# Optimization experiments

Hardware: AMD Instinct MI355X
Metric: run time of the kernel (lower is better)

The kernel has to match this reference:

```python
import jax, jax.numpy as jnp
import numpy as np

HEADS = 16
DIM_HEAD = 64


def rotate_half(t):
    x1, x2 = jnp.split(t, 2, axis=-1)
    return jnp.concatenate((-x2, x1), axis=-1)


def apply_rotary_pos_emb(t, freqs):
    # t: [b, h, n, l], freqs: [n, l]
    seq_len = t.shape[-2]
    freqs = freqs[-seq_len:, :]
    return t * jnp.cos(freqs) + rotate_half(t) * jnp.sin(freqs)


def setup_inputs() -> dict:
    key = jax.random.key(0)
    ks = jax.random.split(key, 6)
    b, n, dim, l = 2, 2048, 1024, 32
    x = jax.random.normal(ks[0], (b, n, dim), dtype=jnp.float32)
    rotary_pos_emb = jax.random.normal(ks[1], (n, l), dtype=jnp.float32)
    s = 0.02
    Wq = jax.random.normal(ks[2], (dim, dim), dtype=jnp.float32) * s
    Wk = jax.random.normal(ks[3], (dim, dim), dtype=jnp.float32) * s
    Wv = jax.random.normal(ks[4], (dim, dim), dtype=jnp.float32) * s
    Wout = jax.random.normal(ks[5], (dim, dim), dtype=jnp.float32) * s
    return {"x": x, "rotary_pos_emb": rotary_pos_emb, "Wq": Wq, "Wk": Wk, "Wv": Wv, "Wout": Wout}


def reference(x, rotary_pos_emb, Wq, Wk, Wv, Wout):
    b, n, _ = x.shape
    h, d = HEADS, DIM_HEAD
    scale = d ** -0.5

    def to_heads(t):
        return t.reshape(b, n, h, d).transpose(0, 2, 1, 3)  # b h n d

    q = to_heads(x @ Wq)
    k = to_heads(x @ Wk)
    v = to_heads(x @ Wv)

    # partial rotary on first l dims of q, k, v (module applies rope to v too)
    l = rotary_pos_emb.shape[-1]

    def rope(t):
        tl, tr = t[..., :l], t[..., l:]
        return jnp.concatenate((apply_rotary_pos_emb(tl, rotary_pos_emb), tr), axis=-1)

    q, k, v = rope(q), rope(k), rope(v)

    dots = jnp.einsum('bhid,bhjd->bhij', q, k) * scale  # [b, h, n, n]
    mask_value = jnp.finfo(dots.dtype).min
    causal = jnp.triu(jnp.ones((n, n), dtype=bool), k=1)  # i < j
    dots = jnp.where(causal[None, None, :, :], mask_value, dots)

    attn = jax.nn.softmax(dots, axis=-1)
    out = jnp.einsum('bhij,bhjd->bhid', attn, v)
    out = out.transpose(0, 2, 1, 3).reshape(b, n, h * d)  # b n (h d)
    return out @ Wout
```

## Files before the change

kernel.cpp:

```cpp
#include <hip/hip_runtime.h>
#include <hip/hip_bf16.h>
#include <stdint.h>

#define BATCH 2
#define SEQ 2048
#define NHEADS 16
#define DIM 1024
#define MTOT 4096
#define LOG2E 1.4426950408889634f
#define QSCALE (0.125f * LOG2E)
#define DEFER_THR 11.54f

typedef __attribute__((ext_vector_type(8))) short s16x8;
typedef __attribute__((ext_vector_type(4))) float f32x4;
typedef unsigned short u16;

__device__ __forceinline__ u16 f2b(float f) {
  union { float f; uint32_t u; } v; v.f = f;
  uint32_t r = v.u + 0x7FFFu + ((v.u >> 16) & 1u);
  return (u16)(r >> 16);
}
__device__ __forceinline__ u16 f2b_fast(float f) {
  union { float f; uint32_t u; } v; v.f = f;
  return (u16)((v.u + 0x8000u) >> 16);
}
__device__ __forceinline__ float b2f(u16 h) {
  union { uint32_t u; float f; } v; v.u = ((uint32_t)h) << 16;
  return v.f;
}

__device__ __forceinline__ void gload_lds16(void* lds, const void* g) {
  __builtin_amdgcn_global_load_lds(
      (const __attribute__((address_space(1))) unsigned int*)g,
      (__attribute__((address_space(3))) unsigned int*)lds, 16, 0, 0);
}

__global__ __launch_bounds__(256) void prep_kernel(
    const float* __restrict__ x, const float* __restrict__ Wq,
    const float* __restrict__ Wk, const float* __restrict__ Wv,
    const float* __restrict__ Wo, const float* __restrict__ rot,
    u16* __restrict__ xb, u16* __restrict__ WtAll, float2* __restrict__ cs) {
  __shared__ float tile[32][33];
  int bid = blockIdx.x, t = threadIdx.x;
  if (bid < 4096) {
    int i = (bid * 256 + t) * 4;
    float4 v = *(const float4*)(x + i);
    ushort4 o;
    o.x = f2b(v.x); o.y = f2b(v.y); o.z = f2b(v.z); o.w = f2b(v.w);
    *(ushort4*)(xb + i) = o;
  } else if (bid < 8192) {
    int bb = bid - 4096;
    int z = bb >> 10, xB = bb & 31, yB = (bb >> 5) & 31;
    const float* W = (z == 0) ? Wq : (z == 1) ? Wk : (z == 2) ? Wv : Wo;
    u16* Wt = WtAll + (size_t)z * DIM * DIM;
    int k0 = xB * 32, n0 = yB * 32;
    int tx = t & 31, ty = t >> 5;
#pragma unroll
    for (int i = 0; i < 4; i++) {
      int r = ty + i * 8;
      tile[r][tx] = W[(size_t)(k0 + r) * DIM + n0 + tx];
    }
    __syncthreads();
#pragma unroll
    for (int i = 0; i < 4; i++) {
      int r = ty + i * 8;
      Wt[(size_t)(n0 + r) * DIM + k0 + tx] = f2b(tile[tx][r]);
    }
  } else {
    int i = (bid - 8192) * 256 + t;
    float f = rot[i];
    float s, c;
    __sincosf(f, &s, &c);
    cs[i] = make_float2(c, s);
  }
}

#define NKT 16
__global__ __launch_bounds__(512, 2) void qkv8_kernel(
    const u16* __restrict__ A, const u16* __restrict__ Bt,
    const float2* __restrict__ cs, u16* __restrict__ Qh,
    u16* __restrict__ Kh, u16* __restrict__ Vt) {
  __shared__ u16 lds[2][4][8192];
  const int t = threadIdx.x;
  const int w = t >> 6, l = t & 63;
  const int wr = w >> 2, wc = w & 3;
  const int lr = l & 15, lg = l >> 4;
  const int rowBase = blockIdx.x * 256;
  const int colBase = blockIdx.y * 256;
  const char* Ab = (const char*)(A + (size_t)rowBase * DIM);
  const char* Bb = (const char*)(Bt + (size_t)colBase * DIM);
  const int t16 = t * 16;
  const int swz = ((lr >> 1) & 3) << 4;

  f32x4 acc[8][4];
#pragma unroll
  for (int m = 0; m < 8; m++)
#pragma unroll
    for (int n = 0; n < 4; n++) acc[m][n] = (f32x4){0.f, 0.f, 0.f, 0.f};

  auto stageH = [&](int buf, int kind, int kt) {
    const char* gb = (kind >= 2) ? Bb : Ab;
    int khalf = kind & 1;
    char* ldst = (char*)&lds[buf][kind][0];
#pragma unroll
    for (int i = 0; i < 2; i++) {
      int ob = t16 + i * 8192;
      int row = ob >> 6, cb = ob & 63;
      gload_lds16(ldst + ob,
                  gb + (size_t)row * (DIM * 2) + kt * 128 + khalf * 64 +
                      (cb ^ (((row >> 1) & 3) << 4)));
    }
  };
  auto rdA = [&](int cur, int m, int kk) -> s16x8 {
    int R = wr * 128 + m * 16 + lr;
    return *(const s16x8*)((const char*)&lds[cur][kk][0] + R * 64 + ((lg * 16) ^ swz));
  };
  auto rdB = [&](int cur, int n, int kk) -> s16x8 {
    int R = wc * 64 + n * 16 + lr;
    return *(const s16x8*)((const char*)&lds[cur][2 + kk][0] + R * 64 + ((lg * 16) ^ swz));
  };

  stageH(0, 0, 0); stageH(0, 2, 0); stageH(0, 1, 0); stageH(0, 3, 0);
  stageH(1, 2, 1); stageH(1, 0, 1); stageH(1, 3, 1);

  for (int kt = 0; kt < NKT; ++kt) {
    const int cur = kt & 1, nxt = cur ^ 1;
    if (kt >= NKT - 2) { asm volatile("s_waitcnt vmcnt(0)" ::: "memory"); }
    else               { asm volatile("s_waitcnt vmcnt(6)" ::: "memory"); }
    __builtin_amdgcn_s_barrier();
    __builtin_amdgcn_sched_barrier(0);

    s16x8 af[4], bf[4];
#pragma unroll
    for (int i = 0; i < 4; i++) { af[i] = rdA(cur, i, 0); bf[i] = rdB(cur, i, 0); }
    if (kt + 1 < NKT) stageH(nxt, 1, kt + 1);
    __builtin_amdgcn_s_barrier();
    __builtin_amdgcn_sched_barrier(0);
    __builtin_amdgcn_s_setprio(1);
#pragma unroll
    for (int m = 0; m < 4; m++)
#pragma unroll
      for (int n = 0; n < 4; n++)
        acc[m][n] = __builtin_amdgcn_mfma_f32_16x16x32_bf16(af[m], bf[n], acc[m][n], 0, 0, 0);
    __builtin_amdgcn_s_setprio(0);
    __builtin_amdgcn_s_barrier();
    __builtin_amdgcn_sched_barrier(0);
#pragma unroll
    for (int i = 0; i < 4; i++) af[i] = rdA(cur, 4 + i, 0);
    if (kt + 2 < NKT) stageH(cur, 2, kt + 2);
    __builtin_amdgcn_s_barrier();
    __builtin_amdgcn_sched_barrier(0);
    __builtin_amdgcn_s_setprio(1);
#pragma unroll
    for (int m = 0; m < 4; m++)
#pragma unroll
      for (int n = 0; n < 4; n++)
        acc[4 + m][n] = __builtin_amdgcn_mfma_f32_16x16x32_bf16(af[m], bf[n], acc[4 + m][n], 0, 0, 0);
    __builtin_amdgcn_s_setprio(0);
    __builtin_amdgcn_s_barrier();
    __builtin_amdgcn_sched_barrier(0);
#pragma unroll
    for (int i = 0; i < 4; i++) { af[i] = rdA(cur, i, 1); bf[i] = rdB(cur, i, 1); }
    if (kt + 2 < NKT) stageH(cur, 0, kt + 2);
    __builtin_amdgcn_s_barrier();
    __builtin_amdgcn_sched_barrier(0);
    __builtin_amdgcn_s_setprio(1);
#pragma unroll
    for (int m = 0; m < 4; m++)
#pragma unroll
      for (int n = 0; n < 4; n++)
        acc[m][n] = __builtin_amdgcn_mfma_f32_16x16x32_bf16(af[m], bf[n], acc[m][n], 0, 0, 0);
    __builtin_amdgcn_s_setprio(0);
    __builtin_amdgcn_s_barrier();
    __builtin_amdgcn_sched_barrier(0);
#pragma unroll
    for (int i = 0; i < 4; i++) af[i] = rdA(cur, 4 + i, 1);
    if (kt + 2 < NKT) stageH(cur, 3, kt + 2);
    __builtin_amdgcn_s_barrier();
    __builtin_amdgcn_sched_barrier(0);
    __builtin_amdgcn_s_setprio(1);
#pragma unroll
    for (int m = 0; m < 4; m++)
#pragma unroll
      for (int n = 0; n < 4; n++)
        acc[4 + m][n] = __builtin_amdgcn_mfma_f32_16x16x32_bf16(af[m], bf[n], acc[4 + m][n], 0, 0, 0);
    __builtin_amdgcn_s_setprio(0);
    __builtin_amdgcn_s_barrier();
    __builtin_amdgcn_sched_barrier(0);
  }

  int cg = colBase + wc * 64;
  int z = cg >> 10;
  int h = (cg >> 6) & (NHEADS - 1);
  if (z == 2) {
#pragma unroll
    for (int m = 0; m < 8; m++) {
#pragma unroll
      for (int r = 0; r < 4; r++) {
        int row = rowBase + wr * 128 + m * 16 + lg * 4 + r;
        int nrow = row & (SEQ - 1);
        int b2 = row >> 11;
        const float2* csr = cs + (size_t)nrow * 32;
        float a0 = acc[m][0][r], a1 = acc[m][1][r];
        float2 f0 = csr[lr];
        float2 f1 = csr[16 + lr];
        float o0 = a0 * f0.x - a1 * f0.y;
        float o1 = a1 * f1.x + a0 * f1.y;
        size_t vbase = ((size_t)(b2 * NHEADS + h) * 64) * SEQ + nrow;
        Vt[vbase + (size_t)lr * SEQ]        = f2b(o0);
        Vt[vbase + (size_t)(16 + lr) * SEQ] = f2b(o1);
        Vt[vbase + (size_t)(32 + lr) * SEQ] = f2b(acc[m][2][r]);
        Vt[vbase + (size_t)(48 + lr) * SEQ] = f2b(acc[m][3][r]);
      }
    }
  } else {
    u16* C = (z == 0) ? Qh : Kh;
    float sc = (z == 0) ? QSCALE : 1.0f;
#pragma unroll
    for (int m = 0; m < 8; m++) {
#pragma unroll
      for (int r = 0; r < 4; r++) {
        int row = rowBase + wr * 128 + m * 16 + lg * 4 + r;
        int nrow = row & (SEQ - 1);
        int b2 = row >> 11;
        const float2* csr = cs + (size_t)nrow * 32;
        float a0 = acc[m][0][r], a1 = acc[m][1][r];
        float2 f0 = csr[lr];
        float2 f1 = csr[16 + lr];
        float o0 = (a0 * f0.x - a1 * f0.y) * sc;
        float o1 = (a1 * f1.x + a0 * f1.y) * sc;
        size_t base = ((size_t)(b2 * NHEADS + h) * SEQ + nrow) * 64;
        C[base + lr]      = f2b(o0);
        C[base + 16 + lr] = f2b(o1);
        C[base + 32 + lr] = f2b(acc[m][2][r] * sc);
        C[base + 48 + lr] = f2b(acc[m][3][r] * sc);
      }
    }
  }
}

__global__ __launch_bounds__(256) void gemm_out(
    const u16* __restrict__ A, const u16* __restrict__ Bt,
    float* __restrict__ C) {
  __shared__ u16 Asm[2][128 * 32];
  __shared__ u16 Bsm[2][128 * 32];
  int t = threadIdx.x;
  int w = t >> 6, l = t & 63;
  int wr = w >> 1, wc = w & 1;
  int lr = l & 15, lg = l >> 4;
  int rowBase = blockIdx.x * 128;
  int colBase = blockIdx.y * 128;
  const char* Ab = (const char*)(A + (size_t)rowBase * DIM);
  const char* Bb = (const char*)(Bt + (size_t)colBase * DIM);

  f32x4 acc[4][4];
#pragma unroll
  for (int m = 0; m < 4; m++)
#pragma unroll
    for (int n = 0; n < 4; n++) acc[m][n] = (f32x4){0.f, 0.f, 0.f, 0.f};

  auto stage = [&](int buf, int kt) {
#pragma unroll
    for (int i = 0; i < 2; i++) {
      int ob = t * 16 + i * 4096;
      int row = ob >> 6, cb = ob & 63;
      int src = row * (DIM * 2) + kt * 64 + (cb ^ (((row >> 1) & 3) << 4));
      gload_lds16((char*)&Asm[buf][0] + ob, Ab + src);
      gload_lds16((char*)&Bsm[buf][0] + ob, Bb + src);
    }
  };

  stage(0, 0);
  for (int kt = 0; kt < DIM / 32; ++kt) {
    int cur = kt & 1;
    __syncthreads();
    if (kt + 1 < DIM / 32) stage(cur ^ 1, kt + 1);
    const char* ab = (const char*)&Asm[cur][0];
    const char* bb = (const char*)&Bsm[cur][0];
    s16x8 af[4], bf[4];
#pragma unroll
    for (int m = 0; m < 4; m++) {
      int R = wr * 64 + m * 16 + lr;
      af[m] = *(const s16x8*)(ab + R * 64 + ((lg * 16) ^ (((R >> 1) & 3) << 4)));
    }
#pragma unroll
    for (int n = 0; n < 4; n++) {
      int R = wc * 64 + n * 16 + lr;
      bf[n] = *(const s16x8*)(bb + R * 64 + ((lg * 16) ^ (((R >> 1) & 3) << 4)));
    }
    __builtin_amdgcn_s_setprio(1);
#pragma unroll
    for (int m = 0; m < 4; m++)
#pragma unroll
      for (int n = 0; n < 4; n++)
        acc[m][n] = __builtin_amdgcn_mfma_f32_16x16x32_bf16(af[m], bf[n], acc[m][n], 0, 0, 0);
    __builtin_amdgcn_s_setprio(0);
  }

#pragma unroll
  for (int m = 0; m < 4; m++)
#pragma unroll
    for (int n = 0; n < 4; n++) {
      int row = rowBase + wr * 64 + m * 16 + lg * 4;
      int col = colBase + wc * 64 + n * 16 + lr;
#pragma unroll
      for (int r = 0; r < 4; r++)
        C[(size_t)(row + r) * DIM + col] = acc[m][n][r];
    }
}

__global__ __launch_bounds__(256) void attn_kernel(
    const u16* __restrict__ Qh, const u16* __restrict__ Kh,
    const u16* __restrict__ Vtg, u16* __restrict__ Ob) {
  int id = blockIdx.x;
  int xcd = id & 7, within = id >> 3;
  int bh = xcd * 4 + (within >> 4);
  int pi = within & 15;
  int b = bh >> 4, h = bh & 15;
  __shared__ u16 Ks[2][64 * 64];
  __shared__ u16 Vs[2][64 * 64];
  __shared__ u16 Ps[4][16 * 64];
  int t = threadIdx.x, w = t >> 6, l = t & 63;
  int lr = l & 15, lg = l >> 4;
  char* psb = (char*)&Ps[w][0];

  const char* Kbh = (const char*)(Kh + (size_t)bh * SEQ * 64);
  const char* Vbh = (const char*)Vtg + (size_t)bh * 64 * SEQ * 2;
  const u16* Qbh = Qh + (size_t)bh * SEQ * 64;

  auto stage = [&](int buf, int kt) {
    const char* kg = Kbh + (size_t)kt * 64 * 128;
    const char* vg = Vbh + kt * 128;
#pragma unroll
    for (int i = 0; i < 2; i++) {
      int ob = i * 4096 + t * 16;
      int row = ob >> 7, cb = ob & 127;
      int sw = cb ^ ((row & 7) << 4);
      gload_lds16((char*)&Ks[buf][0] + ob, kg + row * 128 + sw);
      gload_lds16((char*)&Vs[buf][0] + ob, vg + row * 4096 + sw);
    }
  };

#pragma unroll 1
  for (int ph = 0; ph < 2; ++ph) {
    int qt = ph ? (31 - pi) : pi;
    int nkt = qt + 1;
    int qrow0 = qt * 64 + w * 16;

    s16x8 qf[2];
#pragma unroll
    for (int kk = 0; kk < 2; kk++)
      qf[kk] = *(const s16x8*)(Qbh + (size_t)(qrow0 + lr) * 64 + kk * 32 + lg * 8);

    f32x4 o[4];
#pragma unroll
    for (int n = 0; n < 4; n++) o[n] = (f32x4){0.f, 0.f, 0.f, 0.f};
    float mrun[4], lsum[4];
#pragma unroll
    for (int r = 0; r < 4; r++) { mrun[r] = -3.0e38f; lsum[r] = 0.f; }

    __syncthreads();
    stage(0, 0);
    for (int kt = 0; kt < nkt; ++kt) {
      int cur = kt & 1;
      __syncthreads();
      if (kt + 1 < nkt) stage(cur ^ 1, kt + 1);
      const char* kb = (const char*)&Ks[cur][0];
      const char* vb = (const char*)&Vs[cur][0];

      f32x4 s[4];
#pragma unroll
      for (int n = 0; n < 4; n++) s[n] = (f32x4){0.f, 0.f, 0.f, 0.f};
      __builtin_amdgcn_s_setprio(1);
#pragma unroll
      for (int n = 0; n < 4; n++)
#pragma unroll
        for (int kk = 0; kk < 2; kk++) {
          int R = n * 16 + lr;
          s16x8 bk = *(const s16x8*)(kb + R * 128 + ((kk * 64 + lg * 16) ^ ((R & 7) << 4)));
          s[n] = __builtin_amdgcn_mfma_f32_16x16x32_bf16(qf[kk], bk, s[n], 0, 0, 0);
        }
      __builtin_amdgcn_s_setprio(0);

      if (kt == nkt - 1) {
#pragma unroll
        for (int n = 0; n < 4; n++) {
          int colg = kt * 64 + n * 16 + lr;
#pragma unroll
          for (int r = 0; r < 4; r++) {
            int rowg = qt * 64 + w * 16 + lg * 4 + r;
            if (colg > rowg) s[n][r] = -3.0e38f;
          }
        }
      }

      float tl[4];
#pragma unroll
      for (int r = 0; r < 4; r++)
        tl[r] = fmaxf(fmaxf(s[0][r], s[1][r]), fmaxf(s[2][r], s[3][r]));
      float need = fmaxf(fmaxf(tl[0] - mrun[0], tl[1] - mrun[1]),
                         fmaxf(tl[2] - mrun[2], tl[3] - mrun[3]));
      if (!__all(need <= DEFER_THR)) {
        float tm[4];
#pragma unroll
        for (int r = 0; r < 4; r++) tm[r] = tl[r];
#pragma unroll
        for (int off = 1; off < 16; off <<= 1)
#pragma unroll
          for (int r = 0; r < 4; r++) tm[r] = fmaxf(tm[r], __shfl_xor(tm[r], off, 64));
        float alpha[4];
#pragma unroll
        for (int r = 0; r < 4; r++) {
          float mn = fmaxf(mrun[r], tm[r]);
          alpha[r] = exp2f(mrun[r] - mn);
          mrun[r] = mn;
          lsum[r] *= alpha[r];
        }
#pragma unroll
        for (int n = 0; n < 4; n++)
#pragma unroll
          for (int r = 0; r < 4; r++) o[n][r] *= alpha[r];
      }
#pragma unroll
      for (int n = 0; n < 4; n++) {
#pragma unroll
        for (int r = 0; r < 4; r++) {
          float p = exp2f(s[n][r] - mrun[r]);
          lsum[r] += p;
          int prow = lg * 4 + r;
          *(u16*)(psb + prow * 128 + (((n * 16 + lr) * 2) ^ ((prow & 7) << 4))) = f2b_fast(p);
        }
      }

      s16x8 pa[2];
#pragma unroll
      for (int kk = 0; kk < 2; kk++)
        pa[kk] = *(const s16x8*)(psb + lr * 128 + ((kk * 64 + lg * 16) ^ ((lr & 7) << 4)));
      __builtin_amdgcn_s_setprio(1);
#pragma unroll
      for (int n = 0; n < 4; n++)
#pragma unroll
        for (int kk = 0; kk < 2; kk++) {
          int R = n * 16 + lr;
          s16x8 vv = *(const s16x8*)(vb + R * 128 + ((kk * 64 + lg * 16) ^ ((R & 7) << 4)));
          o[n] = __builtin_amdgcn_mfma_f32_16x16x32_bf16(pa[kk], vv, o[n], 0, 0, 0);
        }
      __builtin_amdgcn_s_setprio(0);
    }

#pragma unroll
    for (int off = 1; off < 16; off <<= 1)
#pragma unroll
      for (int r = 0; r < 4; r++) lsum[r] += __shfl_xor(lsum[r], off, 64);
    float inv[4];
#pragma unroll
    for (int r = 0; r < 4; r++) inv[r] = 1.0f / lsum[r];
#pragma unroll
    for (int n = 0; n < 4; n++)
#pragma unroll
      for (int r = 0; r < 4; r++) {
        int rowg = qt * 64 + w * 16 + lg * 4 + r;
        int col = h * 64 + n * 16 + lr;
        Ob[((size_t)b * SEQ + rowg) * DIM + col] = f2b(o[n][r] * inv[r]);
      }
  }
}

extern "C" void kernel_launch(void* const* d_in, const int* in_sizes, int n_in,
                              void* d_out, int out_size, void* d_ws, size_t ws_size,
                              hipStream_t stream) {
  (void)in_sizes; (void)n_in; (void)out_size; (void)ws_size;
  const float* x = (const float*)d_in[0];
  const float* rot = (const float*)d_in[1];
  const float* Wq = (const float*)d_in[2];
  const float* Wk = (const float*)d_in[3];
  const float* Wv = (const float*)d_in[4];
  const float* Wo = (const float*)d_in[5];

  char* ws = (char*)d_ws;
  u16* xb    = (u16*)(ws);
  u16* WtAll = (u16*)(ws + (8ll << 20));
  u16* Qh    = (u16*)(ws + (16ll << 20));
  u16* Kh    = (u16*)(ws + (24ll << 20));
  u16* Vt    = (u16*)(ws + (32ll << 20));
  u16* Ob    = (u16*)(ws + (40ll << 20));
  float2* cs = (float2*)(ws + (48ll << 20));

  prep_kernel<<<8448, 256, 0, stream>>>(x, Wq, Wk, Wv, Wo, rot, xb, WtAll, cs);
  qkv8_kernel<<<dim3(16, 12), 512, 0, stream>>>(xb, WtAll, cs, Qh, Kh, Vt);
  attn_kernel<<<512, 256, 0, stream>>>(Qh, Kh, Vt, Ob);
  gemm_out<<<dim3(32, 8), 256, 0, stream>>>(Ob, WtAll + 3ll * DIM * DIM, (float*)d_out);
}
```

Before: 199.5 us.

## Compute transposed scores in attention to keep P in registers; halve out-GEMM row tile

The attention kernel now computes S^T (K as the A operand), so each lane holds scores for a single query row. The row max and sum then need only two cross-lane shuffles, and P can be packed with v_cvt_pk_bf16 and fed straight into 16x16x16 MFMAs against V without the LDS round-trip. This drops the per-wave P shared buffer and its writes, reads and swizzle math, at the cost of twice as many smaller MFMAs for the PV product. The output GEMM tile shrinks from 128x128 to 64x128, doubling the grid to 512 blocks to fill more CUs, which trades away some operand reuse.

```diff
diff --git a/kernel.cpp b/kernel.cpp
--- a/kernel.cpp
+++ b/kernel.cpp
@@ -12,6 +12,7 @@
 #define DEFER_THR 11.54f
 
 typedef __attribute__((ext_vector_type(8))) short s16x8;
+typedef __attribute__((ext_vector_type(4))) short s16x4;
 typedef __attribute__((ext_vector_type(4))) float f32x4;
 typedef unsigned short u16;
 
@@ -20,13 +21,14 @@
   uint32_t r = v.u + 0x7FFFu + ((v.u >> 16) & 1u);
   return (u16)(r >> 16);
 }
-__device__ __forceinline__ u16 f2b_fast(float f) {
-  union { float f; uint32_t u; } v; v.f = f;
-  return (u16)((v.u + 0x8000u) >> 16);
-}
 __device__ __forceinline__ float b2f(u16 h) {
   union { uint32_t u; float f; } v; v.u = ((uint32_t)h) << 16;
   return v.f;
+}
+__device__ __forceinline__ uint32_t cvtpk_bf16(float a, float b) {
+  uint32_t r;
+  asm("v_cvt_pk_bf16_f32 %0, %1, %2" : "=v"(r) : "v"(a), "v"(b));
+  return r;
 }
 
 __device__ __forceinline__ void gload_lds16(void* lds, const void* g) {
@@ -242,31 +244,36 @@
 __global__ __launch_bounds__(256) void gemm_out(
     const u16* __restrict__ A, const u16* __restrict__ Bt,
     float* __restrict__ C) {
-  __shared__ u16 Asm[2][128 * 32];
+  __shared__ u16 Asm[2][64 * 32];
   __shared__ u16 Bsm[2][128 * 32];
   int t = threadIdx.x;
   int w = t >> 6, l = t & 63;
   int wr = w >> 1, wc = w & 1;
   int lr = l & 15, lg = l >> 4;
-  int rowBase = blockIdx.x * 128;
+  int rowBase = blockIdx.x * 64;
   int colBase = blockIdx.y * 128;
   const char* Ab = (const char*)(A + (size_t)rowBase * DIM);
   const char* Bb = (const char*)(Bt + (size_t)colBase * DIM);
 
-  f32x4 acc[4][4];
-#pragma unroll
-  for (int m = 0; m < 4; m++)
+  f32x4 acc[2][4];
+#pragma unroll
+  for (int m = 0; m < 2; m++)
 #pragma unroll
     for (int n = 0; n < 4; n++) acc[m][n] = (f32x4){0.f, 0.f, 0.f, 0.f};
 
   auto stage = [&](int buf, int kt) {
+    {
+      int ob = t * 16;
+      int row = ob >> 6, cb = ob & 63;
+      gload_lds16((char*)&Asm[buf][0] + ob,
+                  Ab + (size_t)row * (DIM * 2) + kt * 64 + (cb ^ (((row >> 1) & 3) << 4)));
+    }
 #pragma unroll
     for (int i = 0; i < 2; i++) {
       int ob = t * 16 + i * 4096;
       int row = ob >> 6, cb = ob & 63;
-      int src = row * (DIM * 2) + kt * 64 + (cb ^ (((row >> 1) & 3) << 4));
-      gload_lds16((char*)&Asm[buf][0] + ob, Ab + src);
-      gload_lds16((char*)&Bsm[buf][0] + ob, Bb + src);
+      gload_lds16((char*)&Bsm[buf][0] + ob,
+                  Bb + (size_t)row * (DIM * 2) + kt * 64 + (cb ^ (((row >> 1) & 3) << 4)));
     }
   };
 
@@ -277,10 +284,10 @@
     if (kt + 1 < DIM / 32) stage(cur ^ 1, kt + 1);
     const char* ab = (const char*)&Asm[cur][0];
     const char* bb = (const char*)&Bsm[cur][0];
-    s16x8 af[4], bf[4];
-#pragma unroll
-    for (int m = 0; m < 4; m++) {
-      int R = wr * 64 + m * 16 + lr;
+    s16x8 af[2], bf[4];
+#pragma unroll
+    for (int m = 0; m < 2; m++) {
+      int R = wr * 32 + m * 16 + lr;
       af[m] = *(const s16x8*)(ab + R * 64 + ((lg * 16) ^ (((R >> 1) & 3) << 4)));
     }
 #pragma unroll
@@ -290,7 +297,7 @@
     }
     __builtin_amdgcn_s_setprio(1);
 #pragma unroll
-    for (int m = 0; m < 4; m++)
+    for (int m = 0; m < 2; m++)
 #pragma unroll
       for (int n = 0; n < 4; n++)
         acc[m][n] = __builtin_amdgcn_mfma_f32_16x16x32_bf16(af[m], bf[n], acc[m][n], 0, 0, 0);
@@ -298,10 +305,10 @@
   }
 
 #pragma unroll
-  for (int m = 0; m < 4; m++)
+  for (int m = 0; m < 2; m++)
 #pragma unroll
     for (int n = 0; n < 4; n++) {
-      int row = rowBase + wr * 64 + m * 16 + lg * 4;
+      int row = rowBase + wr * 32 + m * 16 + lg * 4;
       int col = colBase + wc * 64 + n * 16 + lr;
 #pragma unroll
       for (int r = 0; r < 4; r++)
@@ -319,10 +326,8 @@
   int b = bh >> 4, h = bh & 15;
   __shared__ u16 Ks[2][64 * 64];
   __shared__ u16 Vs[2][64 * 64];
-  __shared__ u16 Ps[4][16 * 64];
   int t = threadIdx.x, w = t >> 6, l = t & 63;
   int lr = l & 15, lg = l >> 4;
-  char* psb = (char*)&Ps[w][0];
 
   const char* Kbh = (const char*)(Kh + (size_t)bh * SEQ * 64);
   const char* Vbh = (const char*)Vtg + (size_t)bh * 64 * SEQ * 2;
@@ -345,19 +350,17 @@
   for (int ph = 0; ph < 2; ++ph) {
     int qt = ph ? (31 - pi) : pi;
     int nkt = qt + 1;
-    int qrow0 = qt * 64 + w * 16;
+    int qrow = qt * 64 + w * 16 + lr;
 
     s16x8 qf[2];
 #pragma unroll
     for (int kk = 0; kk < 2; kk++)
-      qf[kk] = *(const s16x8*)(Qbh + (size_t)(qrow0 + lr) * 64 + kk * 32 + lg * 8);
+      qf[kk] = *(const s16x8*)(Qbh + (size_t)qrow * 64 + kk * 32 + lg * 8);
 
     f32x4 o[4];
 #pragma unroll
-    for (int n = 0; n < 4; n++) o[n] = (f32x4){0.f, 0.f, 0.f, 0.f};
-    float mrun[4], lsum[4];
-#pragma unroll
-    for (int r = 0; r < 4; r++) { mrun[r] = -3.0e38f; lsum[r] = 0.f; }
+    for (int dt = 0; dt < 4; dt++) o[dt] = (f32x4){0.f, 0.f, 0.f, 0.f};
+    float mrun = -3.0e38f, lsum = 0.f;
 
     __syncthreads();
     stage(0, 0);
@@ -377,92 +380,84 @@
 #pragma unroll
         for (int kk = 0; kk < 2; kk++) {
           int R = n * 16 + lr;
-          s16x8 bk = *(const s16x8*)(kb + R * 128 + ((kk * 64 + lg * 16) ^ ((R & 7) << 4)));
-          s[n] = __builtin_amdgcn_mfma_f32_16x16x32_bf16(qf[kk], bk, s[n], 0, 0, 0);
+          s16x8 kf = *(const s16x8*)(kb + R * 128 + ((kk * 64 + lg * 16) ^ ((R & 7) << 4)));
+          s[n] = __builtin_amdgcn_mfma_f32_16x16x32_bf16(kf, qf[kk], s[n], 0, 0, 0);
         }
       __builtin_amdgcn_s_setprio(0);
 
       if (kt == nkt - 1) {
 #pragma unroll
         for (int n = 0; n < 4; n++) {
-          int colg = kt * 64 + n * 16 + lr;
-#pragma unroll
-          for (int r = 0; r < 4; r++) {
-            int rowg = qt * 64 + w * 16 + lg * 4 + r;
-            if (colg > rowg) s[n][r] = -3.0e38f;
-          }
+          int kbase = kt * 64 + n * 16 + lg * 4;
+#pragma unroll
+          for (int r = 0; r < 4; r++)
+            if (kbase + r > qrow) s[n][r] = -3.0e38f;
         }
       }
 
-      float tl[4];
-#pragma unroll
-      for (int r = 0; r < 4; r++)
-        tl[r] = fmaxf(fmaxf(s[0][r], s[1][r]), fmaxf(s[2][r], s[3][r]));
-      float need = fmaxf(fmaxf(tl[0] - mrun[0], tl[1] - mrun[1]),
-                         fmaxf(tl[2] - mrun[2], tl[3] - mrun[3]));
-      if (!__all(need <= DEFER_THR)) {
-        float tm[4];
-#pragma unroll
-        for (int r = 0; r < 4; r++) tm[r] = tl[r];
-#pragma unroll
-        for (int off = 1; off < 16; off <<= 1)
-#pragma unroll
-          for (int r = 0; r < 4; r++) tm[r] = fmaxf(tm[r], __shfl_xor(tm[r], off, 64));
-        float alpha[4];
-#pragma unroll
-        for (int r = 0; r < 4; r++) {
-          float mn = fmaxf(mrun[r], tm[r]);
-          alpha[r] = exp2f(mrun[r] - mn);
-          mrun[r] = mn;
-          lsum[r] *= alpha[r];
+      float mloc;
+      {
+        float m0 = fmaxf(fmaxf(s[0][0], s[0][1]), fmaxf(s[0][2], s[0][3]));
+        float m1 = fmaxf(fmaxf(s[1][0], s[1][1]), fmaxf(s[1][2], s[1][3]));
+        float m2 = fmaxf(fmaxf(s[2][0], s[2][1]), fmaxf(s[2][2], s[2][3]));
+        float m3 = fmaxf(fmaxf(s[3][0], s[3][1]), fmaxf(s[3][2], s[3][3]));
+        mloc = fmaxf(fmaxf(m0, m1), fmaxf(m2, m3));
+      }
+      mloc = fmaxf(mloc, __shfl_xor(mloc, 16, 64));
+      mloc = fmaxf(mloc, __shfl_xor(mloc, 32, 64));
+      if (!__all(mloc - mrun <= DEFER_THR)) {
+        float mn = fmaxf(mrun, mloc);
+        float alpha = exp2f(mrun - mn);
+        mrun = mn; lsum *= alpha;
+#pragma unroll
+        for (int dt = 0; dt < 4; dt++)
+#pragma unroll
+          for (int r = 0; r < 4; r++) o[dt][r] *= alpha;
+      }
+      float p[4][4];
+#pragma unroll
+      for (int n = 0; n < 4; n++)
+#pragma unroll
+        for (int r = 0; r < 4; r++) p[n][r] = exp2f(s[n][r] - mrun);
+      lsum += ((p[0][0] + p[0][1]) + (p[0][2] + p[0][3])) +
+              ((p[1][0] + p[1][1]) + (p[1][2] + p[1][3])) +
+              ((p[2][0] + p[2][1]) + (p[2][2] + p[2][3])) +
+              ((p[3][0] + p[3][1]) + (p[3][2] + p[3][3]));
+
+      s16x4 pb[4];
+#pragma unroll
+      for (int n = 0; n < 4; n++) {
+        union { uint32_t u[2]; s16x4 v; } pu;
+        pu.u[0] = cvtpk_bf16(p[n][0], p[n][1]);
+        pu.u[1] = cvtpk_bf16(p[n][2], p[n][3]);
+        pb[n] = pu.v;
+      }
+
+      __builtin_amdgcn_s_setprio(1);
+#pragma unroll
+      for (int dt = 0; dt < 4; dt++) {
+        int R = dt * 16 + lr;
+#pragma unroll
+        for (int n = 0; n < 4; n++) {
+          s16x4 vf = *(const s16x4*)(vb + R * 128 + ((n * 32 + lg * 8) ^ ((R & 7) << 4)));
+          o[dt] = __builtin_amdgcn_mfma_f32_16x16x16bf16_1k(vf, pb[n], o[dt], 0, 0, 0);
         }
-#pragma unroll
-        for (int n = 0; n < 4; n++)
-#pragma unroll
-          for (int r = 0; r < 4; r++) o[n][r] *= alpha[r];
-      }
-#pragma unroll
-      for (int n = 0; n < 4; n++) {
-#pragma unroll
-        for (int r = 0; r < 4; r++) {
-          float p = exp2f(s[n][r] - mrun[r]);
-          lsum[r] += p;
-          int prow = lg * 4 + r;
-          *(u16*)(psb + prow * 128 + (((n * 16 + lr) * 2) ^ ((prow & 7) << 4))) = f2b_fast(p);
-        }
-      }
-
-      s16x8 pa[2];
-#pragma unroll
-      for (int kk = 0; kk < 2; kk++)
-        pa[kk] = *(const s16x8*)(psb + lr * 128 + ((kk * 64 + lg * 16) ^ ((lr & 7) << 4)));
-      __builtin_amdgcn_s_setprio(1);
-#pragma unroll
-      for (int n = 0; n < 4; n++)
-#pragma unroll
-        for (int kk = 0; kk < 2; kk++) {
-          int R = n * 16 + lr;
-          s16x8 vv = *(const s16x8*)(vb + R * 128 + ((kk * 64 + lg * 16) ^ ((R & 7) << 4)));
-          o[n] = __builtin_amdgcn_mfma_f32_16x16x32_bf16(pa[kk], vv, o[n], 0, 0, 0);
-        }
+      }
       __builtin_amdgcn_s_setprio(0);
     }
 
-#pragma unroll
-    for (int off = 1; off < 16; off <<= 1)
-#pragma unroll
-      for (int r = 0; r < 4; r++) lsum[r] += __shfl_xor(lsum[r], off, 64);
-    float inv[4];
-#pragma unroll
-    for (int r = 0; r < 4; r++) inv[r] = 1.0f / lsum[r];
-#pragma unroll
-    for (int n = 0; n < 4; n++)
-#pragma unroll
-      for (int r = 0; r < 4; r++) {
-        int rowg = qt * 64 + w * 16 + lg * 4 + r;
-        int col = h * 64 + n * 16 + lr;
-        Ob[((size_t)b * SEQ + rowg) * DIM + col] = f2b(o[n][r] * inv[r]);
-      }
+    float sum = lsum;
+    sum += __shfl_xor(sum, 16, 64);
+    sum += __shfl_xor(sum, 32, 64);
+    float inv = 1.0f / sum;
+    u16* orow = Ob + ((size_t)b * SEQ + qrow) * DIM + h * 64 + lg * 4;
+#pragma unroll
+    for (int dt = 0; dt < 4; dt++) {
+      ushort4 ov;
+      ov.x = f2b(o[dt][0] * inv); ov.y = f2b(o[dt][1] * inv);
+      ov.z = f2b(o[dt][2] * inv); ov.w = f2b(o[dt][3] * inv);
+      *(ushort4*)(orow + dt * 16) = ov;
+    }
   }
 }
 
@@ -489,5 +484,5 @@
   prep_kernel<<<8448, 256, 0, stream>>>(x, Wq, Wk, Wv, Wo, rot, xb, WtAll, cs);
   qkv8_kernel<<<dim3(16, 12), 512, 0, stream>>>(xb, WtAll, cs, Qh, Kh, Vt);
   attn_kernel<<<512, 256, 0, stream>>>(Qh, Kh, Vt, Ob);
-  gemm_out<<<dim3(32, 8), 256, 0, stream>>>(Ob, WtAll + 3ll * DIM * DIM, (float*)d_out);
-}
+  gemm_out<<<dim3(64, 8), 256, 0, stream>>>(Ob, WtAll + 3ll * DIM * DIM, (float*)d_out);
+}
```

Result: no change. 200.2 us (+0.4%).
